# Kernel tuning notes

Hardware: AMD Instinct MI355X
Metric: run time of the kernel (lower is better)

The kernel has to match this reference:

```python
import jax, jax.numpy as jnp
import numpy as np
import math

B, LQ, LK = 4, 1024, 2048
QD, KD, VD = 768, 512, 512
H, NH = 1024, 16
HD = H // NH

def setup_inputs() -> dict:
    key = jax.random.key(0)
    ks = jax.random.split(key, 11)
    s = 0.02
    return {
        "query": jax.random.normal(ks[0], (B, LQ, QD), jnp.float32),
        "key": jax.random.normal(ks[1], (B, LK, KD), jnp.float32),
        "value": jax.random.normal(ks[2], (B, LK, VD), jnp.float32),
        "Wq": jax.random.normal(ks[3], (QD, H), jnp.float32) * s,
        "bq": jnp.zeros((H,), jnp.float32),
        "Wk": jax.random.normal(ks[4], (KD, H), jnp.float32) * s,
        "bk": jnp.zeros((H,), jnp.float32),
        "Wv": jax.random.normal(ks[5], (VD, H), jnp.float32) * s,
        "bv": jnp.zeros((H,), jnp.float32),
        "Wo": jax.random.normal(ks[6], (H, H), jnp.float32) * s,
        "bo": jnp.zeros((H,), jnp.float32),
    }

def reference(query, key, value, Wq, bq, Wk, bk, Wv, bv, Wo, bo):
    # project and split heads: [B, L, H] -> [B, NH, L, HD]
    def heads(x):
        b, l, _ = x.shape
        return x.reshape(b, l, NH, HD).transpose(0, 2, 1, 3)
    q = heads(query @ Wq + bq)   # [B, NH, LQ, HD]
    k = heads(key @ Wk + bk)     # [B, NH, LK, HD]
    v = heads(value @ Wv + bv)   # [B, NH, LK, HD]
    scores = jnp.einsum('bhqd,bhkd->bhqk', q, k) / math.sqrt(HD)
    weights = jax.nn.softmax(scores, axis=-1)  # dropout inactive (eval / rate used deterministically as identity)
    att = jnp.einsum('bhqk,bhkd->bhqd', weights, v)
    att = att.transpose(0, 2, 1, 3).reshape(query.shape[0], -1, H)
    out = att @ Wo + bo
    return out
```

## Files before the change

kernel.cpp:

```cpp
#include <hip/hip_runtime.h>
#include <math.h>

using bf16x8 = __attribute__((ext_vector_type(8))) short;
using f32x4  = __attribute__((ext_vector_type(4))) float;
using u32x2  = __attribute__((ext_vector_type(2))) unsigned int;

namespace {
constexpr int kB  = 4;
constexpr int kLQ = 1024;
constexpr int kLK = 2048;
constexpr int kH  = 1024;
constexpr int kHD = 64;
}

__device__ __forceinline__ unsigned short f2bf(float x) {
  union { float f; unsigned int u; } v; v.f = x;
  unsigned int r = v.u + 0x7fffu + ((v.u >> 16) & 1u);
  return (unsigned short)(r >> 16);
}

typedef const __attribute__((address_space(1))) unsigned int guint_t;
typedef __attribute__((address_space(3))) unsigned int luint_t;
__device__ __forceinline__ void g2l16(const void* g, void* l) {
  __builtin_amdgcn_global_load_lds(
      (guint_t*)g,
      (luint_t*)(unsigned int)(unsigned long long)l,
      16, 0, 0);
}

__global__ __launch_bounds__(256) void prep_kernel(
    const float* __restrict__ q, const float* __restrict__ k,
    const float* __restrict__ v, const float* __restrict__ Wq,
    const float* __restrict__ Wk, const float* __restrict__ Wv,
    const float* __restrict__ Wo, unsigned short* __restrict__ qo,
    unsigned short* __restrict__ ko, unsigned short* __restrict__ vo,
    unsigned short* __restrict__ WqT, unsigned short* __restrict__ WkT,
    unsigned short* __restrict__ WvT, unsigned short* __restrict__ WoT)
{
  __shared__ float tile[64][65];
  const int t = threadIdx.x;
  if (blockIdx.x < 5632) {
    int c = blockIdx.x * 256 + t;
    const float* src; unsigned short* dst;
    if (c < 393216)      { src = q; dst = qo; }
    else if (c < 917504) { src = k; dst = ko; c -= 393216; }
    else                 { src = v; dst = vo; c -= 917504; }
    const int i = c * 8;
    const float4 a = *(const float4*)(src + i);
    const float4 b = *(const float4*)(src + i + 4);
    uint4 o;
    o.x = (unsigned int)f2bf(a.x) | ((unsigned int)f2bf(a.y) << 16);
    o.y = (unsigned int)f2bf(a.z) | ((unsigned int)f2bf(a.w) << 16);
    o.z = (unsigned int)f2bf(b.x) | ((unsigned int)f2bf(b.y) << 16);
    o.w = (unsigned int)f2bf(b.z) | ((unsigned int)f2bf(b.w) << 16);
    *(uint4*)(dst + i) = o;
    return;
  }
  int id = blockIdx.x - 5632;
  const float* W; unsigned short* Wt; int Kd;
  if (id < 192)      { W = Wq; Wt = WqT; Kd = 768; }
  else if (id < 320) { W = Wk; Wt = WkT; Kd = 512;  id -= 192; }
  else if (id < 448) { W = Wv; Wt = WvT; Kd = 512;  id -= 320; }
  else               { W = Wo; Wt = WoT; Kd = 1024; id -= 448; }
  const int Nd = 1024;
  const int n0 = (id & 15) * 64;
  const int k0 = (id >> 4) * 64;
  const int rr = t >> 4;
  const int c4 = t & 15;
#pragma unroll
  for (int i = 0; i < 4; ++i) {
    const int row = i * 16 + rr;
    const float4 vv = *(const float4*)(W + (size_t)(k0 + row) * Nd + n0 + c4 * 4);
    tile[row][c4*4+0] = vv.x; tile[row][c4*4+1] = vv.y;
    tile[row][c4*4+2] = vv.z; tile[row][c4*4+3] = vv.w;
  }
  __syncthreads();
#pragma unroll
  for (int i = 0; i < 4; ++i) {
    const int n = i * 16 + rr;
    ushort4 o;
    o.x = f2bf(tile[c4*4+0][n]); o.y = f2bf(tile[c4*4+1][n]);
    o.z = f2bf(tile[c4*4+2][n]); o.w = f2bf(tile[c4*4+3][n]);
    *(ushort4*)(Wt + (size_t)(n0 + n) * Kd + k0 + c4 * 4) = o;
  }
}

__device__ __forceinline__ void gemm_body(
    const unsigned short* __restrict__ A, const unsigned short* __restrict__ Bt,
    const float* __restrict__ bias, void* __restrict__ Cout,
    int N, int K, int bx, int by, int mode, float scale, char* lds)
{
  const int t    = threadIdx.x;
  const int lane = t & 63;
  const int w    = t >> 6;
  const int l15  = lane & 15;
  const int lq8  = (lane >> 4) * 8;
  const int lq4  = (lane >> 4) * 4;
  const int r0   = by * 128;
  const int c0   = bx * 128;
  const int wm   = w >> 1, wn = w & 1;

  f32x4 acc[4][4] = {};

#pragma unroll
  for (int i = 0; i < 4; ++i) {
    const int g = w * 4 + i;
    const unsigned short* src = (g < 8) ? A : Bt;
    const int rbase = (g < 8) ? (r0 + g * 16) : (c0 + (g - 8) * 16);
    g2l16(src + (size_t)(rbase + l15) * K + lq8, lds + g * 1024 + lane * 16);
  }

  int pb = 0;
  for (int k0 = 0; k0 < K; k0 += 32, pb ^= 1) {
    __syncthreads();
    char* buf = lds + pb * 16384;
    if (k0 + 32 < K) {
      char* nbuf = lds + (pb ^ 1) * 16384;
#pragma unroll
      for (int i = 0; i < 4; ++i) {
        const int g = w * 4 + i;
        const unsigned short* src = (g < 8) ? A : Bt;
        const int rbase = (g < 8) ? (r0 + g * 16) : (c0 + (g - 8) * 16);
        g2l16(src + (size_t)(rbase + l15) * K + k0 + 32 + lq8, nbuf + g * 1024 + lane * 16);
      }
    }
    bf16x8 af[4], bfr[4];
#pragma unroll
    for (int i = 0; i < 4; ++i) af[i]  = *(const bf16x8*)(buf + (wm*4 + i) * 1024 + lane * 16);
#pragma unroll
    for (int j = 0; j < 4; ++j) bfr[j] = *(const bf16x8*)(buf + 8192 + (wn*4 + j) * 1024 + lane * 16);
#pragma unroll
    for (int i = 0; i < 4; ++i)
#pragma unroll
      for (int j = 0; j < 4; ++j)
        acc[i][j] = __builtin_amdgcn_mfma_f32_16x16x32_bf16(af[i], bfr[j], acc[i][j], 0, 0, 0);
  }

#pragma unroll
  for (int j = 0; j < 4; ++j) {
    const int col = c0 + wn * 64 + j * 16 + l15;
    const float bcol = bias[col];
#pragma unroll
    for (int i = 0; i < 4; ++i) {
      const int row = r0 + wm * 64 + i * 16 + lq4;
      if (mode == 0) {
        float* out = (float*)Cout;
#pragma unroll
        for (int r = 0; r < 4; ++r) out[(size_t)(row + r) * N + col] = acc[i][j][r] + bcol;
      } else if (mode == 1) {
        unsigned short* out = (unsigned short*)Cout;
#pragma unroll
        for (int r = 0; r < 4; ++r) out[(size_t)(row + r) * N + col] = f2bf((acc[i][j][r] + bcol) * scale);
      } else {
        unsigned short* out = (unsigned short*)Cout;
        const int bb = row >> 11;
        const int lk = row & 2047;
        ushort4 o;
        o.x = f2bf(acc[i][j][0] + bcol); o.y = f2bf(acc[i][j][1] + bcol);
        o.z = f2bf(acc[i][j][2] + bcol); o.w = f2bf(acc[i][j][3] + bcol);
        *(ushort4*)(out + (size_t)(bb * kH + col) * kLK + lk) = o;
      }
    }
  }
}

__global__ __launch_bounds__(256) void qkv_gemm_kernel(
    const unsigned short* __restrict__ qA, const unsigned short* __restrict__ WqT,
    const float* __restrict__ bq, unsigned short* __restrict__ Qb,
    const unsigned short* __restrict__ kA, const unsigned short* __restrict__ WkT,
    const float* __restrict__ bk, unsigned short* __restrict__ Kb,
    const unsigned short* __restrict__ vA, const unsigned short* __restrict__ WvT,
    const float* __restrict__ bv, unsigned short* __restrict__ Vtw)
{
  __shared__ __align__(16) char lds[32768];
  int id = blockIdx.x;
  if (id < 256) {
    gemm_body(qA, WqT, bq, Qb, 1024, 768, id & 7, id >> 3, 1,
              0.18033688011112042f, lds);
  } else if (id < 768) {
    id -= 256;
    gemm_body(kA, WkT, bk, Kb, 1024, 512, id & 7, id >> 3, 1, 1.f, lds);
  } else {
    id -= 768;
    gemm_body(vA, WvT, bv, Vtw, 1024, 512, id & 7, id >> 3, 2, 1.f, lds);
  }
}

__global__ __launch_bounds__(256) void out_gemm_kernel(
    const unsigned short* __restrict__ A, const unsigned short* __restrict__ Bt,
    const float* __restrict__ bias, float* __restrict__ C)
{
  __shared__ __align__(16) char lds[32768];
  gemm_body(A, Bt, bias, C, 1024, 1024, blockIdx.x, blockIdx.y, 0, 1.f, lds);
}

__global__ __launch_bounds__(256) void attn_mfma_kernel(
    const unsigned short* __restrict__ Q, const unsigned short* __restrict__ K,
    const unsigned short* __restrict__ Vt, unsigned short* __restrict__ O)
{
  __shared__ __align__(16) char lds[51200];
  constexpr int POFF = 32768;
  const int t    = threadIdx.x;
  const int lane = t & 63;
  const int w    = t >> 6;
  const int l15  = lane & 15;
  const int lg   = lane >> 4;
  const int lq8  = lg * 8;
  const int lq4  = lg * 4;
  const int flat = blockIdx.x;
  const int bh   = flat & 63;
  const int qb   = flat >> 6;
  const int h    = bh & 15;
  const int b    = bh >> 4;
  const int q0   = qb * 128;
  const int hoff = h * kHD;

  bf16x8 qf[2][2];
#pragma unroll
  for (int qi = 0; qi < 2; ++qi)
#pragma unroll
    for (int kh = 0; kh < 2; ++kh)
      qf[qi][kh] = *(const bf16x8*)(Q + (size_t)(b*kLQ + q0 + w*32 + qi*16 + l15) * kH
                                      + hoff + kh*32 + lq8);

  f32x4 acc[2][4] = {};
  float lsum[2] = {0.f, 0.f};

  char* const pwr = lds + POFF + (w*32 + l15) * 144 + lq4 * 2;
  const char* const prd = lds + POFF + (w*32 + l15) * 144 + lq8 * 2;

#pragma unroll
  for (int i = 0; i < 4; ++i) {
    const int g = w * 4 + i;
    if (g < 8) {
      g2l16(K + (size_t)(b*kLK + (g >> 1)*16 + l15) * kH + hoff + (g & 1)*32 + lq8,
            lds + g * 1024 + lane * 16);
    } else {
      const int gg = g - 8;
      g2l16(Vt + (size_t)(b*kH + hoff + (gg >> 1)*16 + l15) * kLK + (gg & 1)*32 + lq8,
            lds + 8192 + gg * 1024 + lane * 16);
    }
  }

  int pb = 0;
  for (int kt = 0; kt < kLK / 64; ++kt, pb ^= 1) {
    __syncthreads();
    char* buf = lds + pb * 16384;
    if (kt + 1 < kLK / 64) {
      char* nbuf = lds + (pb ^ 1) * 16384;
      const int kc1 = (kt + 1) * 64;
#pragma unroll
      for (int i = 0; i < 4; ++i) {
        const int g = w * 4 + i;
        if (g < 8) {
          g2l16(K + (size_t)(b*kLK + kc1 + (g >> 1)*16 + l15) * kH + hoff + (g & 1)*32 + lq8,
                nbuf + g * 1024 + lane * 16);
        } else {
          const int gg = g - 8;
          g2l16(Vt + (size_t)(b*kH + hoff + (gg >> 1)*16 + l15) * kLK + kc1 + (gg & 1)*32 + lq8,
                nbuf + 8192 + gg * 1024 + lane * 16);
        }
      }
    }

    f32x4 s[2][4];
#pragma unroll
    for (int kcf = 0; kcf < 4; ++kcf) {
      const bf16x8 kf0 = *(const bf16x8*)(buf + (kcf*2 + 0) * 1024 + lane * 16);
      const bf16x8 kf1 = *(const bf16x8*)(buf + (kcf*2 + 1) * 1024 + lane * 16);
#pragma unroll
      for (int qi = 0; qi < 2; ++qi) {
        f32x4 z = {};
        z = __builtin_amdgcn_mfma_f32_16x16x32_bf16(kf0, qf[qi][0], z, 0, 0, 0);
        z = __builtin_amdgcn_mfma_f32_16x16x32_bf16(kf1, qf[qi][1], z, 0, 0, 0);
        s[qi][kcf] = z;
      }
    }

#pragma unroll
    for (int qi = 0; qi < 2; ++qi)
#pragma unroll
      for (int kcf = 0; kcf < 4; ++kcf) {
        const float p0 = __builtin_amdgcn_exp2f(s[qi][kcf][0]);
        const float p1 = __builtin_amdgcn_exp2f(s[qi][kcf][1]);
        const float p2 = __builtin_amdgcn_exp2f(s[qi][kcf][2]);
        const float p3 = __builtin_amdgcn_exp2f(s[qi][kcf][3]);
        lsum[qi] += (p0 + p1) + (p2 + p3);
        u32x2 pw;
        pw.x = __builtin_amdgcn_perm(__float_as_uint(p1), __float_as_uint(p0), 0x07060302u);
        pw.y = __builtin_amdgcn_perm(__float_as_uint(p3), __float_as_uint(p2), 0x07060302u);
        *(u32x2*)(pwr + qi*2304 + kcf*32) = pw;
      }

    bf16x8 pf[2][2];
#pragma unroll
    for (int qi = 0; qi < 2; ++qi)
#pragma unroll
      for (int kq = 0; kq < 2; ++kq)
        pf[qi][kq] = *(const bf16x8*)(prd + qi*2304 + kq*64);
#pragma unroll
    for (int vd = 0; vd < 4; ++vd) {
      const bf16x8 vf0 = *(const bf16x8*)(buf + 8192 + (vd*2 + 0) * 1024 + lane * 16);
      const bf16x8 vf1 = *(const bf16x8*)(buf + 8192 + (vd*2 + 1) * 1024 + lane * 16);
#pragma unroll
      for (int qi = 0; qi < 2; ++qi) {
        acc[qi][vd] = __builtin_amdgcn_mfma_f32_16x16x32_bf16(pf[qi][0], vf0, acc[qi][vd], 0, 0, 0);
        acc[qi][vd] = __builtin_amdgcn_mfma_f32_16x16x32_bf16(pf[qi][1], vf1, acc[qi][vd], 0, 0, 0);
      }
    }
  }

  float rinv[2][4];
#pragma unroll
  for (int qi = 0; qi < 2; ++qi) {
    float v = lsum[qi];
    v += __shfl_xor(v, 16);
    v += __shfl_xor(v, 32);
    v = 1.f / v;
#pragma unroll
    for (int r = 0; r < 4; ++r) rinv[qi][r] = __shfl(v, lq4 + r);
  }
#pragma unroll
  for (int qi = 0; qi < 2; ++qi)
#pragma unroll
    for (int vd = 0; vd < 4; ++vd)
#pragma unroll
      for (int r = 0; r < 4; ++r)
        O[(size_t)(b*kLQ + q0 + w*32 + qi*16 + lq4 + r) * kH + hoff + vd*16 + l15] =
            f2bf(acc[qi][vd][r] * rinv[qi][r]);
}

extern "C" void kernel_launch(void* const* d_in, const int* in_sizes, int n_in,
                              void* d_out, int out_size, void* d_ws, size_t ws_size,
                              hipStream_t stream) {
  (void)in_sizes; (void)n_in; (void)out_size; (void)ws_size;
  const float* query = (const float*)d_in[0];
  const float* key   = (const float*)d_in[1];
  const float* value = (const float*)d_in[2];
  const float* Wq = (const float*)d_in[3];
  const float* bq = (const float*)d_in[4];
  const float* Wk = (const float*)d_in[5];
  const float* bk = (const float*)d_in[6];
  const float* Wv = (const float*)d_in[7];
  const float* bv = (const float*)d_in[8];
  const float* Wo = (const float*)d_in[9];
  const float* bo = (const float*)d_in[10];
  float* out = (float*)d_out;

  unsigned short* ws  = (unsigned short*)d_ws;
  unsigned short* qA  = ws;
  unsigned short* kA  = qA  + 3145728;
  unsigned short* vA  = kA  + 4194304;
  unsigned short* WqT = vA  + 4194304;
  unsigned short* WkT = WqT + 786432;
  unsigned short* WvT = WkT + 524288;
  unsigned short* WoT = WvT + 524288;
  unsigned short* Qb  = WoT + 1048576;
  unsigned short* Kb  = Qb  + 4194304;
  unsigned short* Vtw = Kb  + 8388608;
  unsigned short* Ab  = Vtw + 8388608;

  dim3 blk(256);
  prep_kernel<<<6336, blk, 0, stream>>>(query, key, value, Wq, Wk, Wv, Wo,
                                        qA, kA, vA, WqT, WkT, WvT, WoT);
  qkv_gemm_kernel<<<1280, blk, 0, stream>>>(qA, WqT, bq, Qb,
                                            kA, WkT, bk, Kb,
                                            vA, WvT, bv, Vtw);
  attn_mfma_kernel<<<512, blk, 0, stream>>>(Qb, Kb, Vtw, Ab);
  out_gemm_kernel<<<dim3(8, 32), blk, 0, stream>>>(Ab, WoT, bo, out);
}
```

Before: 240.2 us.

## Widen GEMM tiles to 128x256 with 512-thread blocks sharing the A tile

The projection and output GEMMs now use 512-thread blocks that compute a 128x256 tile. Two 256-thread halves share one LDS-staged A tile and each loads its own 128-column B tile, which cuts redundant A loads and halves the block count. Block IDs are also remapped in an XCD-aware interleave so that neighbouring tiles land on the same chiplet, for better L2 reuse. The cost is more LDS per block (48 KB) and fewer blocks: 128 for the output GEMM on a 256-CU part, which risks underfilling the device.

```diff
diff --git a/kernel.cpp b/kernel.cpp
--- a/kernel.cpp
+++ b/kernel.cpp
@@ -85,10 +85,12 @@
   }
 }
 
-__device__ __forceinline__ void gemm_body(
-    const unsigned short* __restrict__ A, const unsigned short* __restrict__ Bt,
+__device__ __forceinline__ void gemm_body2(
+    const unsigned short* __restrict__ pA,
+    const unsigned short* __restrict__ pB1,
+    const unsigned short* __restrict__ pB2,
     const float* __restrict__ bias, void* __restrict__ Cout,
-    int N, int K, int bx, int by, int mode, float scale, char* lds)
+    int c0, int r0, int N, int K, int mode, float scale, char* lds)
 {
   const int t    = threadIdx.x;
   const int lane = t & 63;
@@ -96,39 +98,40 @@
   const int l15  = lane & 15;
   const int lq8  = (lane >> 4) * 8;
   const int lq4  = (lane >> 4) * 4;
-  const int r0   = by * 128;
-  const int c0   = bx * 128;
-  const int wm   = w >> 1, wn = w & 1;
+  const int p    = w >> 2;
+  const int wm   = (w >> 1) & 1;
+  const int wn   = w & 1;
 
   f32x4 acc[4][4] = {};
 
 #pragma unroll
-  for (int i = 0; i < 4; ++i) {
-    const int g = w * 4 + i;
-    const unsigned short* src = (g < 8) ? A : Bt;
-    const int rbase = (g < 8) ? (r0 + g * 16) : (c0 + (g - 8) * 16);
-    g2l16(src + (size_t)(rbase + l15) * K + lq8, lds + g * 1024 + lane * 16);
-  }
-
+  for (int i = 0; i < 3; ++i) {
+    const int g = w * 3 + i;
+    const unsigned short* src = (g < 8) ? pA : (g < 16 ? pB1 : pB2);
+    const int sub = g & 7;
+    g2l16(src + (size_t)(sub * 16 + l15) * K + lq8, lds + g * 1024 + lane * 16);
+  }
+
+  const int bbase = 8192 + p * 8192;
   int pb = 0;
   for (int k0 = 0; k0 < K; k0 += 32, pb ^= 1) {
     __syncthreads();
-    char* buf = lds + pb * 16384;
+    char* buf = lds + pb * 24576;
     if (k0 + 32 < K) {
-      char* nbuf = lds + (pb ^ 1) * 16384;
-#pragma unroll
-      for (int i = 0; i < 4; ++i) {
-        const int g = w * 4 + i;
-        const unsigned short* src = (g < 8) ? A : Bt;
-        const int rbase = (g < 8) ? (r0 + g * 16) : (c0 + (g - 8) * 16);
-        g2l16(src + (size_t)(rbase + l15) * K + k0 + 32 + lq8, nbuf + g * 1024 + lane * 16);
+      char* nbuf = lds + (pb ^ 1) * 24576;
+#pragma unroll
+      for (int i = 0; i < 3; ++i) {
+        const int g = w * 3 + i;
+        const unsigned short* src = (g < 8) ? pA : (g < 16 ? pB1 : pB2);
+        const int sub = g & 7;
+        g2l16(src + (size_t)(sub * 16 + l15) * K + k0 + 32 + lq8, nbuf + g * 1024 + lane * 16);
       }
     }
     bf16x8 af[4], bfr[4];
 #pragma unroll
     for (int i = 0; i < 4; ++i) af[i]  = *(const bf16x8*)(buf + (wm*4 + i) * 1024 + lane * 16);
 #pragma unroll
-    for (int j = 0; j < 4; ++j) bfr[j] = *(const bf16x8*)(buf + 8192 + (wn*4 + j) * 1024 + lane * 16);
+    for (int j = 0; j < 4; ++j) bfr[j] = *(const bf16x8*)(buf + bbase + (wn*4 + j) * 1024 + lane * 16);
 #pragma unroll
     for (int i = 0; i < 4; ++i)
 #pragma unroll
@@ -138,7 +141,7 @@
 
 #pragma unroll
   for (int j = 0; j < 4; ++j) {
-    const int col = c0 + wn * 64 + j * 16 + l15;
+    const int col = c0 + p * 128 + wn * 64 + j * 16 + l15;
     const float bcol = bias[col];
 #pragma unroll
     for (int i = 0; i < 4; ++i) {
@@ -164,7 +167,7 @@
   }
 }
 
-__global__ __launch_bounds__(256) void qkv_gemm_kernel(
+__global__ __launch_bounds__(512, 4) void qkv_gemm_kernel(
     const unsigned short* __restrict__ qA, const unsigned short* __restrict__ WqT,
     const float* __restrict__ bq, unsigned short* __restrict__ Qb,
     const unsigned short* __restrict__ kA, const unsigned short* __restrict__ WkT,
@@ -172,26 +175,44 @@
     const unsigned short* __restrict__ vA, const unsigned short* __restrict__ WvT,
     const float* __restrict__ bv, unsigned short* __restrict__ Vtw)
 {
-  __shared__ __align__(16) char lds[32768];
-  int id = blockIdx.x;
-  if (id < 256) {
-    gemm_body(qA, WqT, bq, Qb, 1024, 768, id & 7, id >> 3, 1,
-              0.18033688011112042f, lds);
-  } else if (id < 768) {
-    id -= 256;
-    gemm_body(kA, WkT, bk, Kb, 1024, 512, id & 7, id >> 3, 1, 1.f, lds);
+  __shared__ __align__(16) char lds[49152];
+  const int bid = blockIdx.x;
+  const int lg = (bid & 7) * 80 + (bid >> 3);
+  if (lg < 128) {
+    const int bx = lg & 3, by = lg >> 2;
+    const int r0 = by * 128, c0 = bx * 256;
+    gemm_body2(qA + (size_t)r0 * 768,
+               WqT + (size_t)c0 * 768, WqT + (size_t)(c0 + 128) * 768,
+               bq, Qb, c0, r0, 1024, 768, 1, 0.18033688011112042f, lds);
+  } else if (lg < 384) {
+    const int id = lg - 128;
+    const int bx = id & 3, by = id >> 2;
+    const int r0 = by * 128, c0 = bx * 256;
+    gemm_body2(kA + (size_t)r0 * 512,
+               WkT + (size_t)c0 * 512, WkT + (size_t)(c0 + 128) * 512,
+               bk, Kb, c0, r0, 1024, 512, 1, 1.f, lds);
   } else {
-    id -= 768;
-    gemm_body(vA, WvT, bv, Vtw, 1024, 512, id & 7, id >> 3, 2, 1.f, lds);
-  }
-}
-
-__global__ __launch_bounds__(256) void out_gemm_kernel(
+    const int id = lg - 384;
+    const int bx = id & 3, by = id >> 2;
+    const int r0 = by * 128, c0 = bx * 256;
+    gemm_body2(vA + (size_t)r0 * 512,
+               WvT + (size_t)c0 * 512, WvT + (size_t)(c0 + 128) * 512,
+               bv, Vtw, c0, r0, 1024, 512, 2, 1.f, lds);
+  }
+}
+
+__global__ __launch_bounds__(512, 4) void out_gemm_kernel(
     const unsigned short* __restrict__ A, const unsigned short* __restrict__ Bt,
     const float* __restrict__ bias, float* __restrict__ C)
 {
-  __shared__ __align__(16) char lds[32768];
-  gemm_body(A, Bt, bias, C, 1024, 1024, blockIdx.x, blockIdx.y, 0, 1.f, lds);
+  __shared__ __align__(16) char lds[49152];
+  const int bid = blockIdx.x;
+  const int lg = (bid & 7) * 16 + (bid >> 3);
+  const int bx = lg & 3, by = lg >> 2;
+  const int r0 = by * 128, c0 = bx * 256;
+  gemm_body2(A + (size_t)r0 * 1024,
+             Bt + (size_t)c0 * 1024, Bt + (size_t)(c0 + 128) * 1024,
+             bias, C, c0, r0, 1024, 1024, 0, 1.f, lds);
 }
 
 __global__ __launch_bounds__(256) void attn_mfma_kernel(
@@ -360,12 +381,11 @@
   unsigned short* Vtw = Kb  + 8388608;
   unsigned short* Ab  = Vtw + 8388608;
 
-  dim3 blk(256);
-  prep_kernel<<<6336, blk, 0, stream>>>(query, key, value, Wq, Wk, Wv, Wo,
+  prep_kernel<<<6336, 256, 0, stream>>>(query, key, value, Wq, Wk, Wv, Wo,
                                         qA, kA, vA, WqT, WkT, WvT, WoT);
-  qkv_gemm_kernel<<<1280, blk, 0, stream>>>(qA, WqT, bq, Qb,
-                                            kA, WkT, bk, Kb,
-                                            vA, WvT, bv, Vtw);
-  attn_mfma_kernel<<<512, blk, 0, stream>>>(Qb, Kb, Vtw, Ab);
-  out_gemm_kernel<<<dim3(8, 32), blk, 0, stream>>>(Ab, WoT, bo, out);
-}
+  qkv_gemm_kernel<<<640, 512, 0, stream>>>(qA, WqT, bq, Qb,
+                                           kA, WkT, bk, Kb,
+                                           vA, WvT, bv, Vtw);
+  attn_mfma_kernel<<<512, 256, 0, stream>>>(Qb, Kb, Vtw, Ab);
+  out_gemm_kernel<<<128, 512, 0, stream>>>(Ab, WoT, bo, out);
+}
```

Measured after the change: 261.2 us. +8.7%, slower.
